# Kernel tuning notes

Hardware: AMD Instinct MI355X
Metric: run time of the kernel (lower is better)

## Reference

```python
import jax, jax.numpy as jnp
import numpy as np

N_RAYS, N_SAMPLES, HIDDEN, N_VOXELS = 8192, 256, 64, 1000


def setup_inputs() -> dict:
    key = jax.random.key(0)
    ks = jax.random.split(key, 10)
    ray_start = jax.random.normal(ks[0], (N_RAYS, 3), jnp.float32)
    ray_dir = jax.random.normal(ks[1], (N_RAYS, 3), jnp.float32)
    ray_dir = ray_dir / jnp.linalg.norm(ray_dir, axis=-1, keepdims=True)
    # monotonically increasing depths along each ray
    sampled_depth = jnp.sort(jax.random.uniform(ks[2], (N_RAYS, N_SAMPLES), jnp.float32) * 4.0 + 0.5, axis=-1)
    sampled_dists = jax.random.uniform(ks[3], (N_RAYS, N_SAMPLES), jnp.float32) * 0.02 + 1e-3
    sampled_idx = jax.random.randint(ks[4], (N_RAYS, N_SAMPLES), -333, N_VOXELS).astype(jnp.int64)
    W1 = jax.random.normal(ks[5], (3, HIDDEN), jnp.float32) * 0.5
    b1 = jnp.zeros((HIDDEN,), jnp.float32)
    w_sigma = jax.random.normal(ks[6], (HIDDEN,), jnp.float32) * 0.5
    W_rgb = jax.random.normal(ks[7], (HIDDEN, 3), jnp.float32) * 0.5
    W_dir = jax.random.normal(ks[8], (3, 3), jnp.float32) * 0.5
    b_rgb = jnp.zeros((3,), jnp.float32)
    return {"ray_start": ray_start, "ray_dir": ray_dir, "sampled_depth": sampled_depth,
            "sampled_dists": sampled_dists, "sampled_idx": sampled_idx,
            "W1": W1, "b1": b1, "w_sigma": w_sigma, "W_rgb": W_rgb, "W_dir": W_dir, "b_rgb": b_rgb}


def _volume_render(ray_start, ray_dir, sampled_depth, sampled_dists, sampled_idx,
                   W1, b1, w_sigma, W_rgb, W_dir, b_rgb):
    # sampled_xyz = ray(ray_start, ray_dir, depth)
    xyz = ray_start[:, None, :] + ray_dir[:, None, :] * sampled_depth[..., None]  # [N,P,3]
    h = jax.nn.relu(jnp.einsum('npi,ih->nph', xyz, W1) + b1)                      # [N,P,H]
    sigma = jnp.einsum('nph,h->np', h, w_sigma)                                   # [N,P]
    rgb = jax.nn.sigmoid(jnp.einsum('nph,hc->npc', h, W_rgb)
                         + jnp.einsum('ni,ic->nc', ray_dir, W_dir)[:, None, :] + b_rgb)  # [N,P,3]
    mask = (sampled_idx != -1).astype(sigma.dtype)                                # [N,P]
    # free_energy = relu(sigma) * dists * 7.0, scattered back with zeros at misses
    free_energy = jax.nn.relu(sigma) * sampled_dists * 7.0 * mask
    shifted = jnp.concatenate([jnp.zeros_like(free_energy[:, :1]), free_energy[:, :-1]], axis=-1)
    a = 1.0 - jnp.exp(-free_energy)
    b = jnp.exp(-jnp.cumsum(shifted, axis=-1))
    probs = a * b                                                                 # [N,P]
    depths = jnp.sum(sampled_depth * probs, axis=-1)                              # [N]
    missed = 1.0 - jnp.sum(probs, axis=-1)                                        # [N]
    colors = jnp.sum(rgb * probs[..., None], axis=-2)                             # [N,3]
    return jnp.concatenate([colors, depths[:, None], missed[:, None], probs], axis=-1)  # [N, 3+1+1+P]


def reference(ray_start, ray_dir, sampled_depth, sampled_dists, sampled_idx,
              W1, b1, w_sigma, W_rgb, W_dir, b_rgb):
    return _volume_render(ray_start, ray_dir, sampled_depth, sampled_dists, sampled_idx,
                          W1, b1, w_sigma, W_rgb, W_dir, b_rgb)
```

## Files before the change

kernel.cpp:

```cpp
#include <hip/hip_runtime.h>

#define NRAYS 8192
#define NS    256
#define HID   64
#define RPB   4

__global__ __launch_bounds__(256) void vr_kernel(
    const float* __restrict__ ray_start,
    const float* __restrict__ ray_dir,
    const float* __restrict__ sampled_depth,
    const float* __restrict__ sampled_dists,
    const int*   __restrict__ sampled_idx,
    const float* __restrict__ W1,
    const float* __restrict__ b1,
    const float* __restrict__ w_sigma,
    const float* __restrict__ W_rgb,
    const float* __restrict__ W_dir,
    const float* __restrict__ b_rgb,
    float* __restrict__ out)
{
    __shared__ float4 sWA[HID];
    __shared__ float4 sWB[HID];
    __shared__ float  sWd[12];

    const int t = threadIdx.x;
    if (t < HID) {
        sWA[t] = make_float4(W1[t], W1[HID + t], W1[2*HID + t], b1[t]);
        sWB[t] = make_float4(w_sigma[t], W_rgb[t*3+0], W_rgb[t*3+1], W_rgb[t*3+2]);
    } else if (t < HID + 12) {
        sWd[t - HID] = (t < HID + 9) ? W_dir[t - HID] : b_rgb[t - HID - 9];
    }
    __syncthreads();

    const int lane = t & 63;
    const int wave = t >> 6;
    const int ray  = blockIdx.x * RPB + wave;

    const float ox = ray_start[ray*3+0], oy = ray_start[ray*3+1], oz = ray_start[ray*3+2];
    const float dx = ray_dir[ray*3+0],  dy = ray_dir[ray*3+1],  dz = ray_dir[ray*3+2];

    const float dwr = dx*sWd[0] + dy*sWd[3] + dz*sWd[6] + sWd[9];
    const float dwg = dx*sWd[1] + dy*sWd[4] + dz*sWd[7] + sWd[10];
    const float dwb = dx*sWd[2] + dy*sWd[5] + dz*sWd[8] + sWd[11];

    const size_t rbase = (size_t)ray * NS;
    const float4 dep = ((const float4*)(sampled_depth + rbase))[lane];
    const float4 dst = ((const float4*)(sampled_dists + rbase))[lane];
    const int4   vidx = ((const int4*)(sampled_idx + rbase))[lane];

    const float dpt[4] = {dep.x, dep.y, dep.z, dep.w};
    const float dsv[4] = {dst.x, dst.y, dst.z, dst.w};
    const int   idx4[4] = {vidx.x, vidx.y, vidx.z, vidx.w};

    float X[4], Y[4], Z[4];
#pragma unroll
    for (int j = 0; j < 4; ++j) {
        X[j] = fmaf(dx, dpt[j], ox);
        Y[j] = fmaf(dy, dpt[j], oy);
        Z[j] = fmaf(dz, dpt[j], oz);
    }

    float sig[4] = {0,0,0,0};
    float cr[4]  = {0,0,0,0};
    float cg[4]  = {0,0,0,0};
    float cb[4]  = {0,0,0,0};

#pragma unroll 16
    for (int h = 0; h < HID; ++h) {
        const float4 a = sWA[h];
        const float4 b = sWB[h];
#pragma unroll
        for (int j = 0; j < 4; ++j) {
            float hv = fmaf(a.x, X[j], fmaf(a.y, Y[j], fmaf(a.z, Z[j], a.w)));
            hv = fmaxf(hv, 0.f);
            sig[j] = fmaf(hv, b.x, sig[j]);
            cr[j]  = fmaf(hv, b.y, cr[j]);
            cg[j]  = fmaf(hv, b.z, cg[j]);
            cb[j]  = fmaf(hv, b.w, cb[j]);
        }
    }

    float fe[4], c[4];
#pragma unroll
    for (int j = 0; j < 4; ++j) {
        float f = fmaxf(sig[j], 0.f) * dsv[j] * 7.0f;
        if (idx4[j] == -1) f = 0.f;
        fe[j] = f;
        c[j] = (j == 0) ? f : c[j-1] + f;
    }

    float tot = c[3];
#pragma unroll
    for (int off = 1; off < 64; off <<= 1) {
        float v = __shfl_up(tot, off, 64);
        if (lane >= off) tot += v;
    }
    const float base = tot - c[3];

    float s0 = 0.f, s1 = 0.f, s2 = 0.f, s3 = 0.f, s4 = 0.f;
    float prob[4];
#pragma unroll
    for (int j = 0; j < 4; ++j) {
        const float excl = base + ((j == 0) ? 0.f : c[j-1]);
        const float p = (1.f - __expf(-fe[j])) * __expf(-excl);
        prob[j] = p;
        const float r = __builtin_amdgcn_rcpf(1.f + __expf(-(cr[j] + dwr)));
        const float g = __builtin_amdgcn_rcpf(1.f + __expf(-(cg[j] + dwg)));
        const float b = __builtin_amdgcn_rcpf(1.f + __expf(-(cb[j] + dwb)));
        s0 += p;
        s1 = fmaf(dpt[j], p, s1);
        s2 = fmaf(r, p, s2);
        s3 = fmaf(g, p, s3);
        s4 = fmaf(b, p, s4);
    }

#pragma unroll
    for (int off = 32; off >= 1; off >>= 1) {
        s0 += __shfl_xor(s0, off, 64);
        s1 += __shfl_xor(s1, off, 64);
        s2 += __shfl_xor(s2, off, 64);
        s3 += __shfl_xor(s3, off, 64);
        s4 += __shfl_xor(s4, off, 64);
    }

    float* orow = out + (size_t)ray * (NS + 5);
#pragma unroll
    for (int j = 0; j < 4; ++j)
        orow[5 + 4*lane + j] = prob[j];

    if (lane == 0) {
        orow[0] = s2;
        orow[1] = s3;
        orow[2] = s4;
        orow[3] = s1;
        orow[4] = 1.f - s0;
    }
}

extern "C" void kernel_launch(void* const* d_in, const int* in_sizes, int n_in,
                              void* d_out, int out_size, void* d_ws, size_t ws_size,
                              hipStream_t stream)
{
    vr_kernel<<<NRAYS / RPB, 256, 0, stream>>>(
        (const float*)d_in[0],
        (const float*)d_in[1],
        (const float*)d_in[2],
        (const float*)d_in[3],
        (const int*)  d_in[4],
        (const float*)d_in[5],
        (const float*)d_in[6],
        (const float*)d_in[7],
        (const float*)d_in[8],
        (const float*)d_in[9],
        (const float*)d_in[10],
        (float*)d_out);
}
```

Measured before the change: 118.8 us.

## Fold ray origin into per-ray hidden affine and use packed FMA with readlane weights

Rewrites the hidden-layer pre-activation as A + depth*B, with A and B precomputed per ray and per hidden unit, one unit per lane. This cuts the first layer from three FMAs to one per sample and hidden unit. The per-unit weights are broadcast with readlane instead of LDS loads, which removes the shared-memory staging and the block barrier. The inner math uses two-wide vector FMAs so the compiler can emit packed v_pk_fma_f32 instructions. In exchange there are six readlanes per hidden unit, and full unrolling of 64 iterations raises code size and SGPR pressure.

```diff
diff --git a/kernel.cpp b/kernel.cpp
--- a/kernel.cpp
+++ b/kernel.cpp
@@ -4,6 +4,13 @@
 #define NS    256
 #define HID   64
 #define RPB   4
+
+typedef float v2f __attribute__((ext_vector_type(2)));
+
+static __device__ __forceinline__ float rdlane(float v, int l) {
+    return __uint_as_float(__builtin_amdgcn_readlane(__float_as_uint(v), l));
+}
+static __device__ __forceinline__ v2f splat2(float s) { v2f v; v.x = s; v.y = s; return v; }
 
 __global__ __launch_bounds__(256) void vr_kernel(
     const float* __restrict__ ray_start,
@@ -19,19 +26,7 @@
     const float* __restrict__ b_rgb,
     float* __restrict__ out)
 {
-    __shared__ float4 sWA[HID];
-    __shared__ float4 sWB[HID];
-    __shared__ float  sWd[12];
-
-    const int t = threadIdx.x;
-    if (t < HID) {
-        sWA[t] = make_float4(W1[t], W1[HID + t], W1[2*HID + t], b1[t]);
-        sWB[t] = make_float4(w_sigma[t], W_rgb[t*3+0], W_rgb[t*3+1], W_rgb[t*3+2]);
-    } else if (t < HID + 12) {
-        sWd[t - HID] = (t < HID + 9) ? W_dir[t - HID] : b_rgb[t - HID - 9];
-    }
-    __syncthreads();
-
+    const int t    = threadIdx.x;
     const int lane = t & 63;
     const int wave = t >> 6;
     const int ray  = blockIdx.x * RPB + wave;
@@ -39,46 +34,61 @@
     const float ox = ray_start[ray*3+0], oy = ray_start[ray*3+1], oz = ray_start[ray*3+2];
     const float dx = ray_dir[ray*3+0],  dy = ray_dir[ray*3+1],  dz = ray_dir[ray*3+2];
 
-    const float dwr = dx*sWd[0] + dy*sWd[3] + dz*sWd[6] + sWd[9];
-    const float dwg = dx*sWd[1] + dy*sWd[4] + dz*sWd[7] + sWd[10];
-    const float dwb = dx*sWd[2] + dy*sWd[5] + dz*sWd[8] + sWd[11];
+    const float dwr = dx*W_dir[0] + dy*W_dir[3] + dz*W_dir[6] + b_rgb[0];
+    const float dwg = dx*W_dir[1] + dy*W_dir[4] + dz*W_dir[7] + b_rgb[1];
+    const float dwb = dx*W_dir[2] + dy*W_dir[5] + dz*W_dir[8] + b_rgb[2];
+
+    const float w0 = W1[lane], w1 = W1[HID + lane], w2 = W1[2*HID + lane];
+    const float Av = fmaf(w0, ox, fmaf(w1, oy, fmaf(w2, oz, b1[lane])));
+    const float Bv = fmaf(w0, dx, fmaf(w1, dy, w2*dz));
+    const float sv = w_sigma[lane];
+    const float rv = W_rgb[lane*3+0], gv = W_rgb[lane*3+1], bv = W_rgb[lane*3+2];
 
     const size_t rbase = (size_t)ray * NS;
     const float4 dep = ((const float4*)(sampled_depth + rbase))[lane];
     const float4 dst = ((const float4*)(sampled_dists + rbase))[lane];
-    const int4   vidx = ((const int4*)(sampled_idx + rbase))[lane];
+    const int4  vidx = ((const int4*)(sampled_idx + rbase))[lane];
 
+    v2f d01; d01.x = dep.x; d01.y = dep.y;
+    v2f d23; d23.x = dep.z; d23.y = dep.w;
+
+    const v2f zero2 = splat2(0.f);
+    v2f sig01 = zero2, sig23 = zero2;
+    v2f cr01  = zero2, cr23  = zero2;
+    v2f cg01  = zero2, cg23  = zero2;
+    v2f cb01  = zero2, cb23  = zero2;
+
+#pragma unroll
+    for (int h = 0; h < HID; ++h) {
+        const v2f a2 = splat2(rdlane(Av, h));
+        const v2f b2 = splat2(rdlane(Bv, h));
+        const v2f s2 = splat2(rdlane(sv, h));
+        const v2f r2 = splat2(rdlane(rv, h));
+        const v2f g2 = splat2(rdlane(gv, h));
+        const v2f q2 = splat2(rdlane(bv, h));
+
+        v2f h01 = __builtin_elementwise_fma(d01, b2, a2);
+        v2f h23 = __builtin_elementwise_fma(d23, b2, a2);
+        h01 = __builtin_elementwise_max(h01, zero2);
+        h23 = __builtin_elementwise_max(h23, zero2);
+
+        sig01 = __builtin_elementwise_fma(h01, s2, sig01);
+        sig23 = __builtin_elementwise_fma(h23, s2, sig23);
+        cr01  = __builtin_elementwise_fma(h01, r2, cr01);
+        cr23  = __builtin_elementwise_fma(h23, r2, cr23);
+        cg01  = __builtin_elementwise_fma(h01, g2, cg01);
+        cg23  = __builtin_elementwise_fma(h23, g2, cg23);
+        cb01  = __builtin_elementwise_fma(h01, q2, cb01);
+        cb23  = __builtin_elementwise_fma(h23, q2, cb23);
+    }
+
+    const float sig[4] = {sig01.x, sig01.y, sig23.x, sig23.y};
+    const float cr[4]  = {cr01.x,  cr01.y,  cr23.x,  cr23.y};
+    const float cg[4]  = {cg01.x,  cg01.y,  cg23.x,  cg23.y};
+    const float cb[4]  = {cb01.x,  cb01.y,  cb23.x,  cb23.y};
     const float dpt[4] = {dep.x, dep.y, dep.z, dep.w};
     const float dsv[4] = {dst.x, dst.y, dst.z, dst.w};
-    const int   idx4[4] = {vidx.x, vidx.y, vidx.z, vidx.w};
-
-    float X[4], Y[4], Z[4];
-#pragma unroll
-    for (int j = 0; j < 4; ++j) {
-        X[j] = fmaf(dx, dpt[j], ox);
-        Y[j] = fmaf(dy, dpt[j], oy);
-        Z[j] = fmaf(dz, dpt[j], oz);
-    }
-
-    float sig[4] = {0,0,0,0};
-    float cr[4]  = {0,0,0,0};
-    float cg[4]  = {0,0,0,0};
-    float cb[4]  = {0,0,0,0};
-
-#pragma unroll 16
-    for (int h = 0; h < HID; ++h) {
-        const float4 a = sWA[h];
-        const float4 b = sWB[h];
-#pragma unroll
-        for (int j = 0; j < 4; ++j) {
-            float hv = fmaf(a.x, X[j], fmaf(a.y, Y[j], fmaf(a.z, Z[j], a.w)));
-            hv = fmaxf(hv, 0.f);
-            sig[j] = fmaf(hv, b.x, sig[j]);
-            cr[j]  = fmaf(hv, b.y, cr[j]);
-            cg[j]  = fmaf(hv, b.z, cg[j]);
-            cb[j]  = fmaf(hv, b.w, cb[j]);
-        }
-    }
+    const int  idx4[4] = {vidx.x, vidx.y, vidx.z, vidx.w};
 
     float fe[4], c[4];
 #pragma unroll
```

New measurement: 142.5 us. 19.9% more time.

## Precompute per-ray hidden affine coefficients and process eight samples per thread

Applied to the files above, without the earlier changes.

The first-layer projection is rewritten algebraically: for each ray and hidden unit the block precomputes A = W1·origin + b1 and B = W1·dir in shared memory, so each hidden activation becomes a single FMA on depth instead of three. Each thread now handles eight samples, with half-waves serving one ray and eight rays per block, which halves the shuffle scan and reduction widths. Probabilities are computed as differences of consecutive transmittance exponentials, saving one exp per sample. The trade-offs are a larger shared-memory staging step, more registers per thread, and possible precision loss from subtracting nearly equal exponentials.

```diff
diff --git a/kernel.cpp b/kernel.cpp
--- a/kernel.cpp
+++ b/kernel.cpp
@@ -3,7 +3,8 @@
 #define NRAYS 8192
 #define NS    256
 #define HID   64
-#define RPB   4
+#define RPB   8
+#define SPT   8
 
 __global__ __launch_bounds__(256) void vr_kernel(
     const float* __restrict__ ray_start,
@@ -19,116 +20,122 @@
     const float* __restrict__ b_rgb,
     float* __restrict__ out)
 {
-    __shared__ float4 sWA[HID];
-    __shared__ float4 sWB[HID];
-    __shared__ float  sWd[12];
+    __shared__ float4 sW[HID];
+    __shared__ float2 sAB[RPB][HID];
 
     const int t = threadIdx.x;
-    if (t < HID) {
-        sWA[t] = make_float4(W1[t], W1[HID + t], W1[2*HID + t], b1[t]);
-        sWB[t] = make_float4(w_sigma[t], W_rgb[t*3+0], W_rgb[t*3+1], W_rgb[t*3+2]);
-    } else if (t < HID + 12) {
-        sWd[t - HID] = (t < HID + 9) ? W_dir[t - HID] : b_rgb[t - HID - 9];
+    if (t < HID)
+        sW[t] = make_float4(w_sigma[t], W_rgb[t*3+0], W_rgb[t*3+1], W_rgb[t*3+2]);
+
+#pragma unroll
+    for (int p = 0; p < 2; ++p) {
+        const int idx = t + p * 256;
+        const int r   = idx >> 6;
+        const int h   = idx & 63;
+        const int ray = blockIdx.x * RPB + r;
+        const float ox = ray_start[ray*3+0], oy = ray_start[ray*3+1], oz = ray_start[ray*3+2];
+        const float dx = ray_dir[ray*3+0],  dy = ray_dir[ray*3+1],  dz = ray_dir[ray*3+2];
+        const float w0 = W1[h], w1 = W1[HID + h], w2 = W1[2*HID + h];
+        const float A = fmaf(w0, ox, fmaf(w1, oy, fmaf(w2, oz, b1[h])));
+        const float B = fmaf(w0, dx, fmaf(w1, dy, w2 * dz));
+        sAB[r][h] = make_float2(A, B);
     }
     __syncthreads();
 
     const int lane = t & 63;
     const int wave = t >> 6;
-    const int ray  = blockIdx.x * RPB + wave;
+    const int hl   = lane & 31;
+    const int r    = wave * 2 + (lane >> 5);
+    const int ray  = blockIdx.x * RPB + r;
 
-    const float ox = ray_start[ray*3+0], oy = ray_start[ray*3+1], oz = ray_start[ray*3+2];
-    const float dx = ray_dir[ray*3+0],  dy = ray_dir[ray*3+1],  dz = ray_dir[ray*3+2];
+    const float dx = ray_dir[ray*3+0], dy = ray_dir[ray*3+1], dz = ray_dir[ray*3+2];
+    const float dwr = fmaf(dx, W_dir[0], fmaf(dy, W_dir[3], fmaf(dz, W_dir[6], b_rgb[0])));
+    const float dwg = fmaf(dx, W_dir[1], fmaf(dy, W_dir[4], fmaf(dz, W_dir[7], b_rgb[1])));
+    const float dwb = fmaf(dx, W_dir[2], fmaf(dy, W_dir[5], fmaf(dz, W_dir[8], b_rgb[2])));
 
-    const float dwr = dx*sWd[0] + dy*sWd[3] + dz*sWd[6] + sWd[9];
-    const float dwg = dx*sWd[1] + dy*sWd[4] + dz*sWd[7] + sWd[10];
-    const float dwb = dx*sWd[2] + dy*sWd[5] + dz*sWd[8] + sWd[11];
+    const size_t rbase = (size_t)ray * NS + (size_t)hl * SPT;
+    const float4 dep0 = ((const float4*)(sampled_depth + rbase))[0];
+    const float4 dep1 = ((const float4*)(sampled_depth + rbase))[1];
+    const float4 dst0 = ((const float4*)(sampled_dists + rbase))[0];
+    const float4 dst1 = ((const float4*)(sampled_dists + rbase))[1];
+    const int4   vi0  = ((const int4*)(sampled_idx + rbase))[0];
+    const int4   vi1  = ((const int4*)(sampled_idx + rbase))[1];
 
-    const size_t rbase = (size_t)ray * NS;
-    const float4 dep = ((const float4*)(sampled_depth + rbase))[lane];
-    const float4 dst = ((const float4*)(sampled_dists + rbase))[lane];
-    const int4   vidx = ((const int4*)(sampled_idx + rbase))[lane];
+    const float dpt[SPT] = {dep0.x, dep0.y, dep0.z, dep0.w, dep1.x, dep1.y, dep1.z, dep1.w};
+    const float dsv[SPT] = {dst0.x, dst0.y, dst0.z, dst0.w, dst1.x, dst1.y, dst1.z, dst1.w};
+    const int   vid[SPT] = {vi0.x, vi0.y, vi0.z, vi0.w, vi1.x, vi1.y, vi1.z, vi1.w};
 
-    const float dpt[4] = {dep.x, dep.y, dep.z, dep.w};
-    const float dsv[4] = {dst.x, dst.y, dst.z, dst.w};
-    const int   idx4[4] = {vidx.x, vidx.y, vidx.z, vidx.w};
+    float sig[SPT] = {0,0,0,0,0,0,0,0};
+    float cr[SPT]  = {0,0,0,0,0,0,0,0};
+    float cg[SPT]  = {0,0,0,0,0,0,0,0};
+    float cb[SPT]  = {0,0,0,0,0,0,0,0};
 
-    float X[4], Y[4], Z[4];
+#pragma unroll 8
+    for (int h = 0; h < HID; ++h) {
+        const float4 w  = sW[h];
+        const float2 ab = sAB[r][h];
 #pragma unroll
-    for (int j = 0; j < 4; ++j) {
-        X[j] = fmaf(dx, dpt[j], ox);
-        Y[j] = fmaf(dy, dpt[j], oy);
-        Z[j] = fmaf(dz, dpt[j], oz);
-    }
-
-    float sig[4] = {0,0,0,0};
-    float cr[4]  = {0,0,0,0};
-    float cg[4]  = {0,0,0,0};
-    float cb[4]  = {0,0,0,0};
-
-#pragma unroll 16
-    for (int h = 0; h < HID; ++h) {
-        const float4 a = sWA[h];
-        const float4 b = sWB[h];
-#pragma unroll
-        for (int j = 0; j < 4; ++j) {
-            float hv = fmaf(a.x, X[j], fmaf(a.y, Y[j], fmaf(a.z, Z[j], a.w)));
-            hv = fmaxf(hv, 0.f);
-            sig[j] = fmaf(hv, b.x, sig[j]);
-            cr[j]  = fmaf(hv, b.y, cr[j]);
-            cg[j]  = fmaf(hv, b.z, cg[j]);
-            cb[j]  = fmaf(hv, b.w, cb[j]);
+        for (int j = 0; j < SPT; ++j) {
+            const float hv = fmaxf(fmaf(ab.y, dpt[j], ab.x), 0.f);
+            sig[j] = fmaf(hv, w.x, sig[j]);
+            cr[j]  = fmaf(hv, w.y, cr[j]);
+            cg[j]  = fmaf(hv, w.z, cg[j]);
+            cb[j]  = fmaf(hv, w.w, cb[j]);
         }
     }
 
-    float fe[4], c[4];
+    float c[SPT];
+    float run = 0.f;
 #pragma unroll
-    for (int j = 0; j < 4; ++j) {
+    for (int j = 0; j < SPT; ++j) {
         float f = fmaxf(sig[j], 0.f) * dsv[j] * 7.0f;
-        if (idx4[j] == -1) f = 0.f;
-        fe[j] = f;
-        c[j] = (j == 0) ? f : c[j-1] + f;
+        if (vid[j] == -1) f = 0.f;
+        run += f;
+        c[j] = run;
     }
 
-    float tot = c[3];
+    float tot = run;
 #pragma unroll
-    for (int off = 1; off < 64; off <<= 1) {
-        float v = __shfl_up(tot, off, 64);
-        if (lane >= off) tot += v;
+    for (int off = 1; off < 32; off <<= 1) {
+        const float v = __shfl_up(tot, off, 32);
+        if (hl >= off) tot += v;
     }
-    const float base = tot - c[3];
+    const float base = tot - run;
 
+    float Eprev = __expf(-base);
+    float prob[SPT];
     float s0 = 0.f, s1 = 0.f, s2 = 0.f, s3 = 0.f, s4 = 0.f;
-    float prob[4];
 #pragma unroll
-    for (int j = 0; j < 4; ++j) {
-        const float excl = base + ((j == 0) ? 0.f : c[j-1]);
-        const float p = (1.f - __expf(-fe[j])) * __expf(-excl);
+    for (int j = 0; j < SPT; ++j) {
+        const float Ej = __expf(-(base + c[j]));
+        const float p  = Eprev - Ej;
+        Eprev = Ej;
         prob[j] = p;
-        const float r = __builtin_amdgcn_rcpf(1.f + __expf(-(cr[j] + dwr)));
-        const float g = __builtin_amdgcn_rcpf(1.f + __expf(-(cg[j] + dwg)));
-        const float b = __builtin_amdgcn_rcpf(1.f + __expf(-(cb[j] + dwb)));
+        const float rr = __builtin_amdgcn_rcpf(1.f + __expf(-(cr[j] + dwr)));
+        const float gg = __builtin_amdgcn_rcpf(1.f + __expf(-(cg[j] + dwg)));
+        const float bb = __builtin_amdgcn_rcpf(1.f + __expf(-(cb[j] + dwb)));
         s0 += p;
         s1 = fmaf(dpt[j], p, s1);
-        s2 = fmaf(r, p, s2);
-        s3 = fmaf(g, p, s3);
-        s4 = fmaf(b, p, s4);
+        s2 = fmaf(rr, p, s2);
+        s3 = fmaf(gg, p, s3);
+        s4 = fmaf(bb, p, s4);
     }
 
 #pragma unroll
-    for (int off = 32; off >= 1; off >>= 1) {
-        s0 += __shfl_xor(s0, off, 64);
-        s1 += __shfl_xor(s1, off, 64);
-        s2 += __shfl_xor(s2, off, 64);
-        s3 += __shfl_xor(s3, off, 64);
-        s4 += __shfl_xor(s4, off, 64);
+    for (int off = 16; off >= 1; off >>= 1) {
+        s0 += __shfl_xor(s0, off, 32);
+        s1 += __shfl_xor(s1, off, 32);
+        s2 += __shfl_xor(s2, off, 32);
+        s3 += __shfl_xor(s3, off, 32);
+        s4 += __shfl_xor(s4, off, 32);
     }
 
     float* orow = out + (size_t)ray * (NS + 5);
 #pragma unroll
-    for (int j = 0; j < 4; ++j)
-        orow[5 + 4*lane + j] = prob[j];
+    for (int j = 0; j < SPT; ++j)
+        orow[5 + SPT*hl + j] = prob[j];
 
-    if (lane == 0) {
+    if (hl == 0) {
         orow[0] = s2;
         orow[1] = s3;
         orow[2] = s4;
```

Measured after the change: 108.4 us. -8.7%, faster.

## Replace per-sample hidden-layer MLP with piecewise-linear prefix sums over depth

Applied to the files above, without the earlier changes.

Along a ray every hidden unit is a linear function of depth, so it turns on or off at a single breakpoint. Each lane now handles one hidden unit: it binary-searches that breakpoint in the sorted depths and scatters slope and intercept contributions for sigma and rgb into per-ray difference arrays in shared memory with atomics. A wave prefix scan then gives every sample's sigma and rgb logits as a*depth+b, which removes the 64-step per-sample loop. It also writes probs as differences of consecutive transmittances, which can lose accuracy through cancellation, and the order of the atomic adds makes the sums non-deterministic.

```diff
diff --git a/kernel.cpp b/kernel.cpp
--- a/kernel.cpp
+++ b/kernel.cpp
@@ -4,6 +4,7 @@
 #define NS    256
 #define HID   64
 #define RPB   4
+#define NSP   260
 
 __global__ __launch_bounds__(256) void vr_kernel(
     const float* __restrict__ ray_start,
@@ -19,99 +20,156 @@
     const float* __restrict__ b_rgb,
     float* __restrict__ out)
 {
-    __shared__ float4 sWA[HID];
-    __shared__ float4 sWB[HID];
-    __shared__ float  sWd[12];
-
-    const int t = threadIdx.x;
-    if (t < HID) {
-        sWA[t] = make_float4(W1[t], W1[HID + t], W1[2*HID + t], b1[t]);
-        sWB[t] = make_float4(w_sigma[t], W_rgb[t*3+0], W_rgb[t*3+1], W_rgb[t*3+2]);
-    } else if (t < HID + 12) {
-        sWd[t - HID] = (t < HID + 9) ? W_dir[t - HID] : b_rgb[t - HID - 9];
-    }
-    __syncthreads();
-
+    __shared__ __align__(16) float sdep[RPB][NS];
+    __shared__ __align__(16) float diff[RPB][8][NSP];
+
+    const int t    = threadIdx.x;
     const int lane = t & 63;
-    const int wave = t >> 6;
-    const int ray  = blockIdx.x * RPB + wave;
-
-    const float ox = ray_start[ray*3+0], oy = ray_start[ray*3+1], oz = ray_start[ray*3+2];
-    const float dx = ray_dir[ray*3+0],  dy = ray_dir[ray*3+1],  dz = ray_dir[ray*3+2];
-
-    const float dwr = dx*sWd[0] + dy*sWd[3] + dz*sWd[6] + sWd[9];
-    const float dwg = dx*sWd[1] + dy*sWd[4] + dz*sWd[7] + sWd[10];
-    const float dwb = dx*sWd[2] + dy*sWd[5] + dz*sWd[8] + sWd[11];
+    const int wv   = t >> 6;
+    const int ray  = blockIdx.x * RPB + wv;
 
     const size_t rbase = (size_t)ray * NS;
     const float4 dep = ((const float4*)(sampled_depth + rbase))[lane];
     const float4 dst = ((const float4*)(sampled_dists + rbase))[lane];
-    const int4   vidx = ((const int4*)(sampled_idx + rbase))[lane];
+    const int4  vidx = ((const int4*)(sampled_idx + rbase))[lane];
+
+    ((float4*)&sdep[wv][0])[lane] = dep;
+    {
+        float4* dz = (float4*)&diff[wv][0][0];
+        const float4 z4 = make_float4(0.f, 0.f, 0.f, 0.f);
+#pragma unroll
+        for (int i = 0; i < 9; ++i) {
+            const int idx = lane + 64 * i;
+            if (idx < (8 * NSP) / 4) dz[idx] = z4;
+        }
+    }
+    __syncthreads();
+
+    const float ox = ray_start[ray*3+0], oy = ray_start[ray*3+1], oz = ray_start[ray*3+2];
+    const float dxr = ray_dir[ray*3+0], dyr = ray_dir[ray*3+1], dzr = ray_dir[ray*3+2];
+
+    const float dwr = fmaf(dxr, W_dir[0], fmaf(dyr, W_dir[3], fmaf(dzr, W_dir[6], b_rgb[0])));
+    const float dwg = fmaf(dxr, W_dir[1], fmaf(dyr, W_dir[4], fmaf(dzr, W_dir[7], b_rgb[1])));
+    const float dwb = fmaf(dxr, W_dir[2], fmaf(dyr, W_dir[5], fmaf(dzr, W_dir[8], b_rgb[2])));
+
+    {
+        const int h = lane;
+        const float w0 = W1[h], w1 = W1[HID + h], w2 = W1[2*HID + h];
+        const float A = fmaf(w0, ox, fmaf(w1, oy, fmaf(w2, oz, b1[h])));
+        const float B = fmaf(w0, dxr, fmaf(w1, dyr, w2 * dzr));
+        const float ws = w_sigma[h];
+        const float wr = W_rgb[h*3+0], wg = W_rgb[h*3+1], wq = W_rgb[h*3+2];
+        const float v0 = A*ws, v1 = B*ws, v2 = A*wr, v3 = B*wr,
+                    v4 = A*wg, v5 = B*wg, v6 = A*wq, v7 = B*wq;
+        float* dr = &diff[wv][0][0];
+        if (B != 0.f) {
+            const float tk  = -A / B;
+            const bool  pos = (B > 0.f);
+            int k = 0;
+#pragma unroll
+            for (int s = 256; s >= 1; s >>= 1) {
+                const int nk = k + s;
+                if (nk <= NS) {
+                    const float dv = sdep[wv][nk - 1];
+                    const bool  le = pos ? (dv <= tk) : (dv < tk);
+                    if (le) k = nk;
+                }
+            }
+            if (pos) {
+                atomicAdd(dr + 0*NSP + k, v0);
+                atomicAdd(dr + 1*NSP + k, v1);
+                atomicAdd(dr + 2*NSP + k, v2);
+                atomicAdd(dr + 3*NSP + k, v3);
+                atomicAdd(dr + 4*NSP + k, v4);
+                atomicAdd(dr + 5*NSP + k, v5);
+                atomicAdd(dr + 6*NSP + k, v6);
+                atomicAdd(dr + 7*NSP + k, v7);
+            } else {
+                atomicAdd(dr + 0*NSP, v0);
+                atomicAdd(dr + 1*NSP, v1);
+                atomicAdd(dr + 2*NSP, v2);
+                atomicAdd(dr + 3*NSP, v3);
+                atomicAdd(dr + 4*NSP, v4);
+                atomicAdd(dr + 5*NSP, v5);
+                atomicAdd(dr + 6*NSP, v6);
+                atomicAdd(dr + 7*NSP, v7);
+                atomicAdd(dr + 0*NSP + k, -v0);
+                atomicAdd(dr + 1*NSP + k, -v1);
+                atomicAdd(dr + 2*NSP + k, -v2);
+                atomicAdd(dr + 3*NSP + k, -v3);
+                atomicAdd(dr + 4*NSP + k, -v4);
+                atomicAdd(dr + 5*NSP + k, -v5);
+                atomicAdd(dr + 6*NSP + k, -v6);
+                atomicAdd(dr + 7*NSP + k, -v7);
+            }
+        } else if (A > 0.f) {
+            atomicAdd(dr + 0*NSP, v0);
+            atomicAdd(dr + 2*NSP, v2);
+            atomicAdd(dr + 4*NSP, v4);
+            atomicAdd(dr + 6*NSP, v6);
+        }
+    }
+    __syncthreads();
+
+    float ch[8][4];
+#pragma unroll
+    for (int c = 0; c < 8; ++c) {
+        const float4 dv = ((const float4*)&diff[wv][c][0])[lane];
+        const float p0 = dv.x, p1 = p0 + dv.y, p2 = p1 + dv.z, p3 = p2 + dv.w;
+        float incl = p3;
+#pragma unroll
+        for (int off = 1; off < 64; off <<= 1) {
+            const float u = __shfl_up(incl, off, 64);
+            if (lane >= off) incl += u;
+        }
+        const float base = incl - p3;
+        ch[c][0] = base + p0; ch[c][1] = base + p1;
+        ch[c][2] = base + p2; ch[c][3] = base + p3;
+    }
 
     const float dpt[4] = {dep.x, dep.y, dep.z, dep.w};
     const float dsv[4] = {dst.x, dst.y, dst.z, dst.w};
-    const int   idx4[4] = {vidx.x, vidx.y, vidx.z, vidx.w};
-
-    float X[4], Y[4], Z[4];
+    const int  vid[4]  = {vidx.x, vidx.y, vidx.z, vidx.w};
+
+    float crj[4], cgj[4], cbj[4], c4[4];
+    float run = 0.f;
 #pragma unroll
     for (int j = 0; j < 4; ++j) {
-        X[j] = fmaf(dx, dpt[j], ox);
-        Y[j] = fmaf(dy, dpt[j], oy);
-        Z[j] = fmaf(dz, dpt[j], oz);
-    }
-
-    float sig[4] = {0,0,0,0};
-    float cr[4]  = {0,0,0,0};
-    float cg[4]  = {0,0,0,0};
-    float cb[4]  = {0,0,0,0};
-
-#pragma unroll 16
-    for (int h = 0; h < HID; ++h) {
-        const float4 a = sWA[h];
-        const float4 b = sWB[h];
-#pragma unroll
-        for (int j = 0; j < 4; ++j) {
-            float hv = fmaf(a.x, X[j], fmaf(a.y, Y[j], fmaf(a.z, Z[j], a.w)));
-            hv = fmaxf(hv, 0.f);
-            sig[j] = fmaf(hv, b.x, sig[j]);
-            cr[j]  = fmaf(hv, b.y, cr[j]);
-            cg[j]  = fmaf(hv, b.z, cg[j]);
-            cb[j]  = fmaf(hv, b.w, cb[j]);
-        }
-    }
-
-    float fe[4], c[4];
+        const float sg = fmaf(dpt[j], ch[1][j], ch[0][j]);
+        crj[j] = fmaf(dpt[j], ch[3][j], ch[2][j]);
+        cgj[j] = fmaf(dpt[j], ch[5][j], ch[4][j]);
+        cbj[j] = fmaf(dpt[j], ch[7][j], ch[6][j]);
+        float f = fmaxf(sg, 0.f) * dsv[j] * 7.0f;
+        if (vid[j] == -1) f = 0.f;
+        run += f;
+        c4[j] = run;
+    }
+
+    float tot = run;
+#pragma unroll
+    for (int off = 1; off < 64; off <<= 1) {
+        const float v = __shfl_up(tot, off, 64);
+        if (lane >= off) tot += v;
+    }
+    const float base2 = tot - run;
+
+    float Eprev = __expf(-base2);
+    float prob[4];
+    float s0 = 0.f, s1 = 0.f, s2 = 0.f, s3 = 0.f, s4 = 0.f;
 #pragma unroll
     for (int j = 0; j < 4; ++j) {
-        float f = fmaxf(sig[j], 0.f) * dsv[j] * 7.0f;
-        if (idx4[j] == -1) f = 0.f;
-        fe[j] = f;
-        c[j] = (j == 0) ? f : c[j-1] + f;
-    }
-
-    float tot = c[3];
-#pragma unroll
-    for (int off = 1; off < 64; off <<= 1) {
-        float v = __shfl_up(tot, off, 64);
-        if (lane >= off) tot += v;
-    }
-    const float base = tot - c[3];
-
-    float s0 = 0.f, s1 = 0.f, s2 = 0.f, s3 = 0.f, s4 = 0.f;
-    float prob[4];
-#pragma unroll
-    for (int j = 0; j < 4; ++j) {
-        const float excl = base + ((j == 0) ? 0.f : c[j-1]);
-        const float p = (1.f - __expf(-fe[j])) * __expf(-excl);
+        const float Ej = __expf(-(base2 + c4[j]));
+        const float p  = Eprev - Ej;
+        Eprev = Ej;
         prob[j] = p;
-        const float r = __builtin_amdgcn_rcpf(1.f + __expf(-(cr[j] + dwr)));
-        const float g = __builtin_amdgcn_rcpf(1.f + __expf(-(cg[j] + dwg)));
-        const float b = __builtin_amdgcn_rcpf(1.f + __expf(-(cb[j] + dwb)));
+        const float rr = __builtin_amdgcn_rcpf(1.f + __expf(-(crj[j] + dwr)));
+        const float gg = __builtin_amdgcn_rcpf(1.f + __expf(-(cgj[j] + dwg)));
+        const float bb = __builtin_amdgcn_rcpf(1.f + __expf(-(cbj[j] + dwb)));
         s0 += p;
         s1 = fmaf(dpt[j], p, s1);
-        s2 = fmaf(r, p, s2);
-        s3 = fmaf(g, p, s3);
-        s4 = fmaf(b, p, s4);
+        s2 = fmaf(rr, p, s2);
+        s3 = fmaf(gg, p, s3);
+        s4 = fmaf(bb, p, s4);
     }
 
 #pragma unroll
```

Result: slower. 141.8 us (+19.4%).
